# Kernel optimization log

Hardware: AMD Instinct MI355X
Metric: run time of the kernel (lower is better)

The kernel has to match this reference:

```python
import jax, jax.numpy as jnp
import numpy as np

D_MODEL = 1024
N_HEADS = 16
D_K = D_MODEL // N_HEADS


def setup_inputs() -> dict:
    key = jax.random.key(0)
    ks = jax.random.split(key, 12)
    B, S, D, H = 2, 2048, D_MODEL, N_HEADS
    s = 1.0 / np.sqrt(D)
    inp = {
        "x": jax.random.normal(ks[0], (B, S, D), jnp.float32),
        "Wq": jax.random.normal(ks[1], (D, D), jnp.float32) * s,
        "bq": jnp.zeros((D,), jnp.float32),
        "Wk": jax.random.normal(ks[2], (D, D), jnp.float32) * s,
        "bk": jnp.zeros((D,), jnp.float32),
        "Wv": jax.random.normal(ks[3], (D, D), jnp.float32) * s,
        "bv": jnp.zeros((D,), jnp.float32),
        "Wo": jax.random.normal(ks[4], (D, D), jnp.float32) * s,
        "bo": jnp.zeros((D,), jnp.float32),
        "Wp": jax.random.normal(ks[5], (D, H), jnp.float32) * s,
        "bp": jnp.zeros((H,), jnp.float32),
        "alpha": jax.random.normal(ks[6], (H,), jnp.float32) * 0.1,
    }
    return inp


def reference(x, Wq, bq, Wk, bk, Wv, bv, Wo, bo, Wp, bp, alpha):
    B, S, D = x.shape
    H, dk = N_HEADS, D_K
    scale = dk ** -0.5
    # projections -> (B, H, S, dk)
    Q = (x @ Wq + bq).reshape(B, S, H, dk).transpose(0, 2, 1, 3)
    K = (x @ Wk + bk).reshape(B, S, H, dk).transpose(0, 2, 1, 3)
    V = (x @ Wv + bv).reshape(B, S, H, dk).transpose(0, 2, 1, 3)
    scores = jnp.einsum("bhid,bhjd->bhij", Q, K) * scale  # (B,H,S,S)
    # phase derived from x: (B,S,H) -> (B,H,S)
    phase = (x @ Wp + bp).transpose(0, 2, 1)
    # coherence(i,j) = cos(phi_i - phi_j), per batch/head
    coherence = jnp.cos(phase[:, :, :, None] - phase[:, :, None, :])
    scores = scores + alpha[None, :, None, None] * coherence
    attn = jax.nn.softmax(scores, axis=-1)
    out = jnp.einsum("bhij,bhjd->bhid", attn, V)  # (B,H,S,dk)
    out = out.transpose(0, 2, 1, 3).reshape(B, S, D)
    return out @ Wo + bo
```

## Files before the change

kernel.cpp:

```cpp
#include <hip/hip_runtime.h>
#include <math.h>


#define S_LEN 2048
#define NHEADS 16

typedef __attribute__((ext_vector_type(8))) short short8;
typedef __attribute__((ext_vector_type(4))) float floatx4;
typedef __attribute__((ext_vector_type(4))) unsigned int uintx4;

__device__ inline unsigned short f2bf(float f) {
    union { float f; unsigned int i; } v; v.f = f;
    unsigned int u = v.i;
    return (unsigned short)((u + 0x7fffu + ((u >> 16) & 1u)) >> 16);
}
__device__ inline unsigned int pack2_bf16(float hi, float lo) {
    union { float f; unsigned int u; } a, b; a.f = hi; b.f = lo;
    return __builtin_amdgcn_perm(a.u, b.u, 0x07060302u);
}
__device__ inline void async_copy16(const unsigned short* src, unsigned short* dst_lds) {
    __builtin_amdgcn_global_load_lds(
        (const __attribute__((address_space(1))) unsigned int*)(src),
        (__attribute__((address_space(3))) unsigned int*)(dst_lds), 16, 0, 0);
}
__device__ inline void async_copy4(const float* src, float* dst_lds) {
    __builtin_amdgcn_global_load_lds(
        (const __attribute__((address_space(1))) unsigned int*)(src),
        (__attribute__((address_space(3))) unsigned int*)(dst_lds), 4, 0, 0);
}

__global__ __launch_bounds__(256) void transpose4(
    const float* __restrict__ w0, const float* __restrict__ w1,
    const float* __restrict__ w2, const float* __restrict__ w3,
    unsigned short* __restrict__ d0, unsigned short* __restrict__ d1,
    unsigned short* __restrict__ d2, unsigned short* __restrict__ d3) {
    __shared__ __align__(16) unsigned short tile[64][72];
    int bid = blockIdx.x;
    int mat = bid >> 8;
    int tl  = bid & 255;
    int tr = tl >> 4, tc = tl & 15;
    const float* src    = (mat == 0) ? w0 : (mat == 1) ? w1 : (mat == 2) ? w2 : w3;
    unsigned short* dst = (mat == 0) ? d0 : (mat == 1) ? d1 : (mat == 2) ? d2 : d3;
    int t = threadIdx.x;
    int col = t & 63, rbase = (t >> 6) * 16;
#pragma unroll
    for (int i = 0; i < 16; i++) {
        int row = rbase + i;
        tile[row][col] = f2bf(src[(size_t)(tr * 64 + row) * 1024 + tc * 64 + col]);
    }
    __syncthreads();
#pragma unroll
    for (int i = 0; i < 16; i++) {
        int row = rbase + i;
        dst[(size_t)(tc * 64 + row) * 1024 + tr * 64 + col] = tile[col][row];
    }
}

__global__ __launch_bounds__(256) void phase_cvt(
    const float* __restrict__ x, const float* __restrict__ Wp,
    const float* __restrict__ bp,
    float* __restrict__ cosP, float* __restrict__ sinP,
    unsigned short* __restrict__ xb) {
    __shared__ float red[256];
    int bid = blockIdx.x;
    int b = bid >> 11, s = bid & 2047;
    int t = threadIdx.x;
    int h = t & 15, c = t >> 4;
    const float* xr = x + (size_t)bid * 1024;
    {
        float4 xv = *reinterpret_cast<const float4*>(&xr[t * 4]);
        uint2 o;
        o.x = (unsigned int)f2bf(xv.x) | ((unsigned int)f2bf(xv.y) << 16);
        o.y = (unsigned int)f2bf(xv.z) | ((unsigned int)f2bf(xv.w) << 16);
        *reinterpret_cast<uint2*>(&xb[(size_t)bid * 1024 + t * 4]) = o;
    }
    float acc = 0.f;
#pragma unroll 8
    for (int kk = 0; kk < 64; kk++) {
        int k = c * 64 + kk;
        acc += xr[k] * Wp[k * 16 + h];
    }
    red[t] = acc;
    __syncthreads();
    if (t < 16) {
        float sum = 0.f;
#pragma unroll
        for (int c2 = 0; c2 < 16; c2++) sum += red[c2 * 16 + t];
        sum += bp[t];
        float sv, cv;
        __sincosf(sum, &sv, &cv);
        size_t o = ((size_t)b * NHEADS + t) * S_LEN + s;
        cosP[o] = cv; sinP[o] = sv;
    }
}

template <int MT>
__global__ __launch_bounds__(256) void gemm_bt(
    const unsigned short* __restrict__ A, const unsigned short* __restrict__ BT,
    int N, int mode,
    const float* __restrict__ b0, const float* __restrict__ b1,
    const float* __restrict__ b2,
    unsigned short* __restrict__ o0, unsigned short* __restrict__ o1,
    unsigned short* __restrict__ o2, float* __restrict__ of) {
    __shared__ __align__(16) unsigned short As[MT * 32];
    __shared__ __align__(16) unsigned short Bs[128 * 32];
    const int K = 1024;
    const int MI = MT / 32;
    int t = threadIdx.x;
    int mBase = blockIdx.x * MT;
    int nBase = blockIdx.y * 128;
    int w = t >> 6, lane = t & 63, l15 = lane & 15, quad = lane >> 4;
    int wm = (w & 1) * (MT / 2), wn = (w >> 1) * 64;
    floatx4 acc[MI][4];
#pragma unroll
    for (int i = 0; i < MI; i++)
#pragma unroll
        for (int j = 0; j < 4; j++) acc[i][j] = (floatx4){0.f, 0.f, 0.f, 0.f};

    int arow = t >> 2, aseg = (t & 3) * 8;
    for (int k0 = 0; k0 < K; k0 += 32) {
        __syncthreads();
#pragma unroll
        for (int i = 0; i < MT / 64; i++)
            async_copy16(&A[(size_t)(mBase + i * 64 + arow) * K + k0 + aseg],
                         &As[(i * 64 + arow) * 32 + aseg]);
#pragma unroll
        for (int i = 0; i < 2; i++)
            async_copy16(&BT[(size_t)(nBase + i * 64 + arow) * K + k0 + aseg],
                         &Bs[(i * 64 + arow) * 32 + aseg]);
        __syncthreads();
        short8 af[MI], bfr[4];
#pragma unroll
        for (int mi = 0; mi < MI; mi++)
            af[mi] = *reinterpret_cast<const short8*>(&As[(wm + mi * 16 + l15) * 32 + quad * 8]);
#pragma unroll
        for (int ni = 0; ni < 4; ni++)
            bfr[ni] = *reinterpret_cast<const short8*>(&Bs[(wn + ni * 16 + l15) * 32 + quad * 8]);
#pragma unroll
        for (int mi = 0; mi < MI; mi++)
#pragma unroll
            for (int ni = 0; ni < 4; ni++)
                acc[mi][ni] = __builtin_amdgcn_mfma_f32_16x16x32_bf16(af[mi], bfr[ni], acc[mi][ni], 0, 0, 0);
    }

#pragma unroll
    for (int mi = 0; mi < MI; mi++) {
        int rowB = mBase + wm + mi * 16 + quad * 4;
#pragma unroll
        for (int ni = 0; ni < 4; ni++) {
            int col = nBase + wn + ni * 16 + l15;
            if (mode == 0) {
                float bias = b0[col];
#pragma unroll
                for (int r = 0; r < 4; r++) {
                    of[(size_t)(rowB + r) * N + col] = acc[mi][ni][r] + bias;
                }
            } else {
                int mat = col >> 10, nn = col & 1023;
                int h = nn >> 6, d = nn & 63;
                int b = rowB >> 11, sidx = rowB & 2047;
                if (mat == 2) {
                    float bv = b2[nn];
                    unsigned int lo = (unsigned int)f2bf(acc[mi][ni][0] + bv) |
                                      ((unsigned int)f2bf(acc[mi][ni][1] + bv) << 16);
                    unsigned int hi = (unsigned int)f2bf(acc[mi][ni][2] + bv) |
                                      ((unsigned int)f2bf(acc[mi][ni][3] + bv) << 16);
                    *reinterpret_cast<uint2*>(
                        &o2[((size_t)((b * NHEADS + h) * 64 + d)) * S_LEN + sidx]) =
                        make_uint2(lo, hi);
                } else {
                    const float* bias  = (mat == 0) ? b0 : b1;
                    unsigned short* op = (mat == 0) ? o0 : o1;
                    float bv = bias[nn];
                    float scl = (mat == 0) ? 0.18033688f : 1.0f;
#pragma unroll
                    for (int r = 0; r < 4; r++) {
                        float cv = (acc[mi][ni][r] + bv) * scl;
                        op[(((size_t)b * NHEADS + h) * S_LEN + (sidx + r)) * 64 + d] = f2bf(cv);
                    }
                }
            }
        }
    }
}

__global__ __launch_bounds__(256) void vtrans(unsigned int* __restrict__ v) {
    __shared__ unsigned int ld[1024];
    size_t base = (size_t)blockIdx.x * 1024;
    int t = threadIdx.x;
    *reinterpret_cast<uintx4*>(&ld[t * 4]) =
        *reinterpret_cast<const uintx4*>(&v[base + t * 4]);
    __syncthreads();
    int tile = t >> 3, m = t & 7;
    int b = ((m >> 2) << 4) + ((m & 3) << 1);
    const unsigned int* tb = &ld[tile * 32];
    unsigned int a0 = tb[b], a1 = tb[b + 1], h0 = tb[b + 8], h1 = tb[b + 9];
    uintx4 o;
    o[0] = __builtin_amdgcn_perm(h0, a0, 0x05040100u);
    o[1] = __builtin_amdgcn_perm(h0, a0, 0x07060302u);
    o[2] = __builtin_amdgcn_perm(h1, a1, 0x05040100u);
    o[3] = __builtin_amdgcn_perm(h1, a1, 0x07060302u);
    *reinterpret_cast<uintx4*>(&v[base + t * 4]) = o;
}

__global__ __launch_bounds__(256) void attn_kernel(
    const unsigned short* __restrict__ Qg, const unsigned short* __restrict__ Kg,
    const unsigned short* __restrict__ VTg,
    const float* __restrict__ cosP, const float* __restrict__ sinP,
    const float* __restrict__ alpha, unsigned short* __restrict__ ctx) {
    __shared__ __align__(16) unsigned short KsB[2][64 * 64];
    __shared__ __align__(16) unsigned short VtB[2][64 * 64];
    __shared__ __align__(16) float csB[2][128];
    __shared__ __align__(16) unsigned short Plb[4][32 * 72];

    int bid = blockIdx.x;
    int bh = bid >> 4, qt = bid & 15;
    int t = threadIdx.x, w = t >> 6, lane = t & 63, l15 = lane & 15, quad = lane >> 4;
    int m0 = qt * 128 + w * 32;
    size_t base = (size_t)bh * (S_LEN * 64);
    size_t phBase = (size_t)bh * S_LEN;
    const float L2E = 1.44269504f;

    int sj = t >> 3, sg = t & 7;
    int srot = ((sg - (sj & 7)) & 7) * 8;

    short8 qf[2][2];
#pragma unroll
    for (int mi = 0; mi < 2; mi++)
#pragma unroll
        for (int c = 0; c < 2; c++)
            qf[mi][c] = *reinterpret_cast<const short8*>(
                &Qg[base + (size_t)(m0 + mi * 16 + l15) * 64 + c * 32 + quad * 8]);

    float alph = alpha[bh & 15] * L2E;
    float ci[2][4], si[2][4];
#pragma unroll
    for (int mi = 0; mi < 2; mi++)
#pragma unroll
        for (int r = 0; r < 4; r++) {
            size_t o = phBase + m0 + mi * 16 + quad * 4 + r;
            ci[mi][r] = alph * cosP[o];
            si[mi][r] = alph * sinP[o];
        }

    {
        async_copy16(&Kg[base + (size_t)(0 * 64 + sj) * 64 + srot], &KsB[0][t * 8]);
        async_copy16(&Kg[base + (size_t)(0 * 64 + sj + 32) * 64 + srot], &KsB[0][2048 + t * 8]);
        async_copy16(&VTg[base + (size_t)sj * S_LEN + 0 * 64 + srot], &VtB[0][t * 8]);
        async_copy16(&VTg[base + (size_t)(sj + 32) * S_LEN + 0 * 64 + srot], &VtB[0][2048 + t * 8]);
        if (w == 0)      async_copy4(&cosP[phBase + 0 * 64 + lane], &csB[0][lane]);
        else if (w == 1) async_copy4(&sinP[phBase + 0 * 64 + lane], &csB[0][64 + lane]);
    }

    floatx4 oacc[2][4], lacc[2];
#pragma unroll
    for (int mi = 0; mi < 2; mi++) {
#pragma unroll
        for (int tt = 0; tt < 4; tt++) oacc[mi][tt] = (floatx4){0.f, 0.f, 0.f, 0.f};
        lacc[mi] = (floatx4){0.f, 0.f, 0.f, 0.f};
    }
    const short8 ones8 = {(short)0x3F80, (short)0x3F80, (short)0x3F80, (short)0x3F80,
                          (short)0x3F80, (short)0x3F80, (short)0x3F80, (short)0x3F80};

    int rot = l15 & 7;
    int cb0 = 16 * ((quad + rot) & 7);
    int cb1 = 16 * ((quad + 4 + rot) & 7);

    for (int kt = 0; kt < 32; kt++) {
        int p = kt & 1;
        __syncthreads();
        if (kt < 31) {
            int kn = kt + 1, pn = p ^ 1;
            async_copy16(&Kg[base + (size_t)(kn * 64 + sj) * 64 + srot], &KsB[pn][t * 8]);
            async_copy16(&Kg[base + (size_t)(kn * 64 + sj + 32) * 64 + srot], &KsB[pn][2048 + t * 8]);
            async_copy16(&VTg[base + (size_t)sj * S_LEN + kn * 64 + srot], &VtB[pn][t * 8]);
            async_copy16(&VTg[base + (size_t)(sj + 32) * S_LEN + kn * 64 + srot], &VtB[pn][2048 + t * 8]);
            if (w == 0)      async_copy4(&cosP[phBase + kn * 64 + lane], &csB[pn][lane]);
            else if (w == 1) async_copy4(&sinP[phBase + kn * 64 + lane], &csB[pn][64 + lane]);
        }

        floatx4 st[2][4];
#pragma unroll
        for (int jt = 0; jt < 4; jt++) {
            const char* kr = (const char*)&KsB[p][(jt * 16 + l15) * 64];
            short8 kf0 = *reinterpret_cast<const short8*>(kr + cb0);
            short8 kf1 = *reinterpret_cast<const short8*>(kr + cb1);
#pragma unroll
            for (int mi = 0; mi < 2; mi++) {
                floatx4 s = (floatx4){0.f, 0.f, 0.f, 0.f};
                s = __builtin_amdgcn_mfma_f32_16x16x32_bf16(qf[mi][0], kf0, s, 0, 0, 0);
                s = __builtin_amdgcn_mfma_f32_16x16x32_bf16(qf[mi][1], kf1, s, 0, 0, 0);
                st[mi][jt] = s;
            }
        }

        float cjv[4], sjv[4];
#pragma unroll
        for (int jt = 0; jt < 4; jt++) {
            cjv[jt] = csB[p][jt * 16 + l15];
            sjv[jt] = csB[p][64 + jt * 16 + l15];
        }

        unsigned int* pl = reinterpret_cast<unsigned int*>(&Plb[w][0]);
#pragma unroll
        for (int mi = 0; mi < 2; mi++)
#pragma unroll
            for (int r = 0; r < 4; r++) {
                float cc = ci[mi][r], ss = si[mi][r];
                float p0 = __builtin_amdgcn_exp2f(st[mi][0][r] + cc * cjv[0] + ss * sjv[0]);
                float p1 = __builtin_amdgcn_exp2f(st[mi][1][r] + cc * cjv[1] + ss * sjv[1]);
                float p2 = __builtin_amdgcn_exp2f(st[mi][2][r] + cc * cjv[2] + ss * sjv[2]);
                float p3 = __builtin_amdgcn_exp2f(st[mi][3][r] + cc * cjv[3] + ss * sjv[3]);
                int row = mi * 16 + quad * 4 + r;
                pl[row * 36 + l15]      = pack2_bf16(p1, p0);
                pl[row * 36 + 16 + l15] = pack2_bf16(p3, p2);
            }

        short8 pf[2][2];
#pragma unroll
        for (int mi = 0; mi < 2; mi++)
#pragma unroll
            for (int c = 0; c < 2; c++)
                pf[mi][c] = *reinterpret_cast<const short8*>(
                    &Plb[w][(mi * 16 + l15) * 72 + c * 32 + quad * 8]);

#pragma unroll
        for (int c = 0; c < 2; c++) {
            int cb = c ? cb1 : cb0;
#pragma unroll
            for (int tt = 0; tt < 4; tt++) {
                const char* vr = (const char*)&VtB[p][(tt * 16 + l15) * 64];
                short8 vf = *reinterpret_cast<const short8*>(vr + cb);
                oacc[0][tt] = __builtin_amdgcn_mfma_f32_16x16x32_bf16(pf[0][c], vf, oacc[0][tt], 0, 0, 0);
                oacc[1][tt] = __builtin_amdgcn_mfma_f32_16x16x32_bf16(pf[1][c], vf, oacc[1][tt], 0, 0, 0);
            }
            lacc[0] = __builtin_amdgcn_mfma_f32_16x16x32_bf16(pf[0][c], ones8, lacc[0], 0, 0, 0);
            lacc[1] = __builtin_amdgcn_mfma_f32_16x16x32_bf16(pf[1][c], ones8, lacc[1], 0, 0, 0);
        }
    }

    int b = bh >> 4, h = bh & 15;
#pragma unroll
    for (int mi = 0; mi < 2; mi++) {
        float inv[4];
#pragma unroll
        for (int r = 0; r < 4; r++) inv[r] = 1.0f / lacc[mi][r];
#pragma unroll
        for (int tt = 0; tt < 4; tt++)
#pragma unroll
            for (int r = 0; r < 4; r++) {
                int srow = m0 + mi * 16 + quad * 4 + r;
                ctx[((size_t)(b * S_LEN + srow)) * 1024 + h * 64 + tt * 16 + l15] =
                    f2bf(oacc[mi][tt][r] * inv[r]);
            }
    }
}

extern "C" void kernel_launch(void* const* d_in, const int* in_sizes, int n_in,
                              void* d_out, int out_size, void* d_ws, size_t ws_size,
                              hipStream_t stream) {
    const float* x     = (const float*)d_in[0];
    const float* Wq    = (const float*)d_in[1];
    const float* bq    = (const float*)d_in[2];
    const float* Wk    = (const float*)d_in[3];
    const float* bk    = (const float*)d_in[4];
    const float* Wv    = (const float*)d_in[5];
    const float* bv    = (const float*)d_in[6];
    const float* Wo    = (const float*)d_in[7];
    const float* bo    = (const float*)d_in[8];
    const float* Wp    = (const float*)d_in[9];
    const float* bp    = (const float*)d_in[10];
    const float* alpha = (const float*)d_in[11];
    float* out = (float*)d_out;

    const size_t MB = 1048576;
    char* ws = (char*)d_ws;
    unsigned short* WT   = (unsigned short*)(ws);
    unsigned short* WoT  = (unsigned short*)(ws + 6 * MB);
    unsigned short* xb   = (unsigned short*)(ws + 8 * MB);
    unsigned short* ctx  = (unsigned short*)(ws + 8 * MB);
    unsigned short* Qw   = (unsigned short*)(ws + 16 * MB);
    unsigned short* Kw   = (unsigned short*)(ws + 24 * MB);
    unsigned short* VTg  = (unsigned short*)(ws + 32 * MB);
    float* cosP          = (float*)(ws + 40 * MB);
    float* sinP          = (float*)(ws + 40 * MB + 262144);

    transpose4<<<dim3(1024), dim3(256), 0, stream>>>(
        Wq, Wk, Wv, Wo, WT, WT + 1048576, WT + 2097152, WoT);
    phase_cvt<<<dim3(4096), dim3(256), 0, stream>>>(
        x, Wp, bp, cosP, sinP, xb);
    gemm_bt<128><<<dim3(32, 24), dim3(256), 0, stream>>>(
        xb, WT, 3072, 1, bq, bk, bv, Qw, Kw, VTg, (float*)nullptr);
    vtrans<<<dim3(2048), dim3(256), 0, stream>>>((unsigned int*)VTg);
    attn_kernel<<<dim3(512), dim3(256), 0, stream>>>(
        Qw, Kw, VTg, cosP, sinP, alpha, ctx);
    gemm_bt<64><<<dim3(64, 8), dim3(256), 0, stream>>>(
        ctx, WoT, 1024, 0, bo, bo, bo,
        (unsigned short*)nullptr, (unsigned short*)nullptr,
        (unsigned short*)nullptr, out);
}
```

Before: 242.5 us.

## Merge prep kernels, fold V permutation into GEMM epilogue, widen attention blocks

Combines the weight transpose and phase/convert kernels into one launch split by block index. The vtrans pass is removed, and the QKV GEMM epilogue now writes V directly in the permuted interleaved layout, using scalar 2-byte stores instead of packed 8-byte stores. The attention kernel moves to 512 threads per block with 8 waves of 16 query rows each instead of 4 waves of 32. This halves per-thread registers and the per-thread async copy count but doubles K/V fragment reads from LDS per query row. The aims are fewer launches, no extra pass over V, and higher occupancy in attention; the cost is scattered V stores and less K/V reuse per wave.

```diff
diff --git a/kernel.cpp b/kernel.cpp
--- a/kernel.cpp
+++ b/kernel.cpp
@@ -29,68 +29,68 @@
         (__attribute__((address_space(3))) unsigned int*)(dst_lds), 4, 0, 0);
 }
 
-__global__ __launch_bounds__(256) void transpose4(
+__global__ __launch_bounds__(256) void prep_kernel(
+    const float* __restrict__ x, const float* __restrict__ Wp,
+    const float* __restrict__ bp,
     const float* __restrict__ w0, const float* __restrict__ w1,
     const float* __restrict__ w2, const float* __restrict__ w3,
     unsigned short* __restrict__ d0, unsigned short* __restrict__ d1,
-    unsigned short* __restrict__ d2, unsigned short* __restrict__ d3) {
-    __shared__ __align__(16) unsigned short tile[64][72];
-    int bid = blockIdx.x;
-    int mat = bid >> 8;
-    int tl  = bid & 255;
-    int tr = tl >> 4, tc = tl & 15;
-    const float* src    = (mat == 0) ? w0 : (mat == 1) ? w1 : (mat == 2) ? w2 : w3;
-    unsigned short* dst = (mat == 0) ? d0 : (mat == 1) ? d1 : (mat == 2) ? d2 : d3;
-    int t = threadIdx.x;
-    int col = t & 63, rbase = (t >> 6) * 16;
-#pragma unroll
-    for (int i = 0; i < 16; i++) {
-        int row = rbase + i;
-        tile[row][col] = f2bf(src[(size_t)(tr * 64 + row) * 1024 + tc * 64 + col]);
-    }
-    __syncthreads();
-#pragma unroll
-    for (int i = 0; i < 16; i++) {
-        int row = rbase + i;
-        dst[(size_t)(tc * 64 + row) * 1024 + tr * 64 + col] = tile[col][row];
-    }
-}
-
-__global__ __launch_bounds__(256) void phase_cvt(
-    const float* __restrict__ x, const float* __restrict__ Wp,
-    const float* __restrict__ bp,
+    unsigned short* __restrict__ d2, unsigned short* __restrict__ d3,
     float* __restrict__ cosP, float* __restrict__ sinP,
     unsigned short* __restrict__ xb) {
-    __shared__ float red[256];
-    int bid = blockIdx.x;
-    int b = bid >> 11, s = bid & 2047;
+    __shared__ __align__(16) unsigned short shmem[64 * 72];
     int t = threadIdx.x;
-    int h = t & 15, c = t >> 4;
-    const float* xr = x + (size_t)bid * 1024;
-    {
-        float4 xv = *reinterpret_cast<const float4*>(&xr[t * 4]);
-        uint2 o;
-        o.x = (unsigned int)f2bf(xv.x) | ((unsigned int)f2bf(xv.y) << 16);
-        o.y = (unsigned int)f2bf(xv.z) | ((unsigned int)f2bf(xv.w) << 16);
-        *reinterpret_cast<uint2*>(&xb[(size_t)bid * 1024 + t * 4]) = o;
-    }
-    float acc = 0.f;
+    if (blockIdx.x < 4096) {
+        float* red = reinterpret_cast<float*>(shmem);
+        int bid = blockIdx.x;
+        int b = bid >> 11, s = bid & 2047;
+        int h = t & 15, c = t >> 4;
+        const float* xr = x + (size_t)bid * 1024;
+        {
+            float4 xv = *reinterpret_cast<const float4*>(&xr[t * 4]);
+            uint2 o;
+            o.x = (unsigned int)f2bf(xv.x) | ((unsigned int)f2bf(xv.y) << 16);
+            o.y = (unsigned int)f2bf(xv.z) | ((unsigned int)f2bf(xv.w) << 16);
+            *reinterpret_cast<uint2*>(&xb[(size_t)bid * 1024 + t * 4]) = o;
+        }
+        float acc = 0.f;
 #pragma unroll 8
-    for (int kk = 0; kk < 64; kk++) {
-        int k = c * 64 + kk;
-        acc += xr[k] * Wp[k * 16 + h];
-    }
-    red[t] = acc;
-    __syncthreads();
-    if (t < 16) {
-        float sum = 0.f;
-#pragma unroll
-        for (int c2 = 0; c2 < 16; c2++) sum += red[c2 * 16 + t];
-        sum += bp[t];
-        float sv, cv;
-        __sincosf(sum, &sv, &cv);
-        size_t o = ((size_t)b * NHEADS + t) * S_LEN + s;
-        cosP[o] = cv; sinP[o] = sv;
+        for (int kk = 0; kk < 64; kk++) {
+            int k = c * 64 + kk;
+            acc += xr[k] * Wp[k * 16 + h];
+        }
+        red[t] = acc;
+        __syncthreads();
+        if (t < 16) {
+            float sum = 0.f;
+#pragma unroll
+            for (int c2 = 0; c2 < 16; c2++) sum += red[c2 * 16 + t];
+            sum += bp[t];
+            float sv, cv;
+            __sincosf(sum, &sv, &cv);
+            size_t o = ((size_t)b * NHEADS + t) * S_LEN + s;
+            cosP[o] = cv; sinP[o] = sv;
+        }
+    } else {
+        unsigned short (*tile)[72] = reinterpret_cast<unsigned short (*)[72]>(shmem);
+        int bid = blockIdx.x - 4096;
+        int mat = bid >> 8;
+        int tl  = bid & 255;
+        int tr = tl >> 4, tc = tl & 15;
+        const float* src    = (mat == 0) ? w0 : (mat == 1) ? w1 : (mat == 2) ? w2 : w3;
+        unsigned short* dst = (mat == 0) ? d0 : (mat == 1) ? d1 : (mat == 2) ? d2 : d3;
+        int col = t & 63, rbase = (t >> 6) * 16;
+#pragma unroll
+        for (int i = 0; i < 16; i++) {
+            int row = rbase + i;
+            tile[row][col] = f2bf(src[(size_t)(tr * 64 + row) * 1024 + tc * 64 + col]);
+        }
+        __syncthreads();
+#pragma unroll
+        for (int i = 0; i < 16; i++) {
+            int row = rbase + i;
+            dst[(size_t)(tc * 64 + row) * 1024 + tr * 64 + col] = tile[col][row];
+        }
     }
 }
 
@@ -161,13 +161,13 @@
                 int b = rowB >> 11, sidx = rowB & 2047;
                 if (mat == 2) {
                     float bv = b2[nn];
-                    unsigned int lo = (unsigned int)f2bf(acc[mi][ni][0] + bv) |
-                                      ((unsigned int)f2bf(acc[mi][ni][1] + bv) << 16);
-                    unsigned int hi = (unsigned int)f2bf(acc[mi][ni][2] + bv) |
-                                      ((unsigned int)f2bf(acc[mi][ni][3] + bv) << 16);
-                    *reinterpret_cast<uint2*>(
-                        &o2[((size_t)((b * NHEADS + h) * 64 + d)) * S_LEN + sidx]) =
-                        make_uint2(lo, hi);
+                    int jj = sidx & 63;
+                    int a2 = jj >> 5, c2 = (jj >> 4) & 1, bb = jj & 15;
+                    size_t rowOff = ((size_t)((b * NHEADS + h) * 64 + d)) * S_LEN +
+                                    (sidx & ~63) + a2 * 32 + c2;
+#pragma unroll
+                    for (int r = 0; r < 4; r++)
+                        o2[rowOff + 2 * (bb + r)] = f2bf(acc[mi][ni][r] + bv);
                 } else {
                     const float* bias  = (mat == 0) ? b0 : b1;
                     unsigned short* op = (mat == 0) ? o0 : o1;
@@ -184,26 +184,7 @@
     }
 }
 
-__global__ __launch_bounds__(256) void vtrans(unsigned int* __restrict__ v) {
-    __shared__ unsigned int ld[1024];
-    size_t base = (size_t)blockIdx.x * 1024;
-    int t = threadIdx.x;
-    *reinterpret_cast<uintx4*>(&ld[t * 4]) =
-        *reinterpret_cast<const uintx4*>(&v[base + t * 4]);
-    __syncthreads();
-    int tile = t >> 3, m = t & 7;
-    int b = ((m >> 2) << 4) + ((m & 3) << 1);
-    const unsigned int* tb = &ld[tile * 32];
-    unsigned int a0 = tb[b], a1 = tb[b + 1], h0 = tb[b + 8], h1 = tb[b + 9];
-    uintx4 o;
-    o[0] = __builtin_amdgcn_perm(h0, a0, 0x05040100u);
-    o[1] = __builtin_amdgcn_perm(h0, a0, 0x07060302u);
-    o[2] = __builtin_amdgcn_perm(h1, a1, 0x05040100u);
-    o[3] = __builtin_amdgcn_perm(h1, a1, 0x07060302u);
-    *reinterpret_cast<uintx4*>(&v[base + t * 4]) = o;
-}
-
-__global__ __launch_bounds__(256) void attn_kernel(
+__global__ __launch_bounds__(512) void attn_kernel(
     const unsigned short* __restrict__ Qg, const unsigned short* __restrict__ Kg,
     const unsigned short* __restrict__ VTg,
     const float* __restrict__ cosP, const float* __restrict__ sinP,
@@ -211,12 +192,12 @@
     __shared__ __align__(16) unsigned short KsB[2][64 * 64];
     __shared__ __align__(16) unsigned short VtB[2][64 * 64];
     __shared__ __align__(16) float csB[2][128];
-    __shared__ __align__(16) unsigned short Plb[4][32 * 72];
+    __shared__ __align__(16) unsigned short Plb[8][16 * 72];
 
     int bid = blockIdx.x;
     int bh = bid >> 4, qt = bid & 15;
     int t = threadIdx.x, w = t >> 6, lane = t & 63, l15 = lane & 15, quad = lane >> 4;
-    int m0 = qt * 128 + w * 32;
+    int m0 = qt * 128 + w * 16;
     size_t base = (size_t)bh * (S_LEN * 64);
     size_t phBase = (size_t)bh * S_LEN;
     const float L2E = 1.44269504f;
@@ -224,41 +205,32 @@
     int sj = t >> 3, sg = t & 7;
     int srot = ((sg - (sj & 7)) & 7) * 8;
 
-    short8 qf[2][2];
-#pragma unroll
-    for (int mi = 0; mi < 2; mi++)
-#pragma unroll
-        for (int c = 0; c < 2; c++)
-            qf[mi][c] = *reinterpret_cast<const short8*>(
-                &Qg[base + (size_t)(m0 + mi * 16 + l15) * 64 + c * 32 + quad * 8]);
+    short8 qf[2];
+#pragma unroll
+    for (int c = 0; c < 2; c++)
+        qf[c] = *reinterpret_cast<const short8*>(
+            &Qg[base + (size_t)(m0 + l15) * 64 + c * 32 + quad * 8]);
 
     float alph = alpha[bh & 15] * L2E;
-    float ci[2][4], si[2][4];
-#pragma unroll
-    for (int mi = 0; mi < 2; mi++)
-#pragma unroll
-        for (int r = 0; r < 4; r++) {
-            size_t o = phBase + m0 + mi * 16 + quad * 4 + r;
-            ci[mi][r] = alph * cosP[o];
-            si[mi][r] = alph * sinP[o];
-        }
+    float ci[4], si[4];
+#pragma unroll
+    for (int r = 0; r < 4; r++) {
+        size_t o = phBase + m0 + quad * 4 + r;
+        ci[r] = alph * cosP[o];
+        si[r] = alph * sinP[o];
+    }
 
     {
-        async_copy16(&Kg[base + (size_t)(0 * 64 + sj) * 64 + srot], &KsB[0][t * 8]);
-        async_copy16(&Kg[base + (size_t)(0 * 64 + sj + 32) * 64 + srot], &KsB[0][2048 + t * 8]);
-        async_copy16(&VTg[base + (size_t)sj * S_LEN + 0 * 64 + srot], &VtB[0][t * 8]);
-        async_copy16(&VTg[base + (size_t)(sj + 32) * S_LEN + 0 * 64 + srot], &VtB[0][2048 + t * 8]);
-        if (w == 0)      async_copy4(&cosP[phBase + 0 * 64 + lane], &csB[0][lane]);
-        else if (w == 1) async_copy4(&sinP[phBase + 0 * 64 + lane], &csB[0][64 + lane]);
-    }
-
-    floatx4 oacc[2][4], lacc[2];
-#pragma unroll
-    for (int mi = 0; mi < 2; mi++) {
-#pragma unroll
-        for (int tt = 0; tt < 4; tt++) oacc[mi][tt] = (floatx4){0.f, 0.f, 0.f, 0.f};
-        lacc[mi] = (floatx4){0.f, 0.f, 0.f, 0.f};
-    }
+        async_copy16(&Kg[base + (size_t)sj * 64 + srot], &KsB[0][t * 8]);
+        async_copy16(&VTg[base + (size_t)sj * S_LEN + srot], &VtB[0][t * 8]);
+        if (w == 2)      async_copy4(&cosP[phBase + lane], &csB[0][lane]);
+        else if (w == 3) async_copy4(&sinP[phBase + lane], &csB[0][64 + lane]);
+    }
+
+    floatx4 oacc[4], lacc;
+#pragma unroll
+    for (int tt = 0; tt < 4; tt++) oacc[tt] = (floatx4){0.f, 0.f, 0.f, 0.f};
+    lacc = (floatx4){0.f, 0.f, 0.f, 0.f};
     const short8 ones8 = {(short)0x3F80, (short)0x3F80, (short)0x3F80, (short)0x3F80,
                           (short)0x3F80, (short)0x3F80, (short)0x3F80, (short)0x3F80};
 
@@ -272,26 +244,21 @@
         if (kt < 31) {
             int kn = kt + 1, pn = p ^ 1;
             async_copy16(&Kg[base + (size_t)(kn * 64 + sj) * 64 + srot], &KsB[pn][t * 8]);
-            async_copy16(&Kg[base + (size_t)(kn * 64 + sj + 32) * 64 + srot], &KsB[pn][2048 + t * 8]);
             async_copy16(&VTg[base + (size_t)sj * S_LEN + kn * 64 + srot], &VtB[pn][t * 8]);
-            async_copy16(&VTg[base + (size_t)(sj + 32) * S_LEN + kn * 64 + srot], &VtB[pn][2048 + t * 8]);
-            if (w == 0)      async_copy4(&cosP[phBase + kn * 64 + lane], &csB[pn][lane]);
-            else if (w == 1) async_copy4(&sinP[phBase + kn * 64 + lane], &csB[pn][64 + lane]);
-        }
-
-        floatx4 st[2][4];
+            if (w == 2)      async_copy4(&cosP[phBase + kn * 64 + lane], &csB[pn][lane]);
+            else if (w == 3) async_copy4(&sinP[phBase + kn * 64 + lane], &csB[pn][64 + lane]);
+        }
+
+        floatx4 st[4];
 #pragma unroll
         for (int jt = 0; jt < 4; jt++) {
             const char* kr = (const char*)&KsB[p][(jt * 16 + l15) * 64];
             short8 kf0 = *reinterpret_cast<const short8*>(kr + cb0);
             short8 kf1 = *reinterpret_cast<const short8*>(kr + cb1);
-#pragma unroll
-            for (int mi = 0; mi < 2; mi++) {
-                floatx4 s = (floatx4){0.f, 0.f, 0.f, 0.f};
-                s = __builtin_amdgcn_mfma_f32_16x16x32_bf16(qf[mi][0], kf0, s, 0, 0, 0);
-                s = __builtin_amdgcn_mfma_f32_16x16x32_bf16(qf[mi][1], kf1, s, 0, 0, 0);
-                st[mi][jt] = s;
-            }
+            floatx4 s = (floatx4){0.f, 0.f, 0.f, 0.f};
+            s = __builtin_amdgcn_mfma_f32_16x16x32_bf16(qf[0], kf0, s, 0, 0, 0);
+            s = __builtin_amdgcn_mfma_f32_16x16x32_bf16(qf[1], kf1, s, 0, 0, 0);
+            st[jt] = s;
         }
 
         float cjv[4], sjv[4];
@@ -303,26 +270,22 @@
 
         unsigned int* pl = reinterpret_cast<unsigned int*>(&Plb[w][0]);
 #pragma unroll
-        for (int mi = 0; mi < 2; mi++)
-#pragma unroll
-            for (int r = 0; r < 4; r++) {
-                float cc = ci[mi][r], ss = si[mi][r];
-                float p0 = __builtin_amdgcn_exp2f(st[mi][0][r] + cc * cjv[0] + ss * sjv[0]);
-                float p1 = __builtin_amdgcn_exp2f(st[mi][1][r] + cc * cjv[1] + ss * sjv[1]);
-                float p2 = __builtin_amdgcn_exp2f(st[mi][2][r] + cc * cjv[2] + ss * sjv[2]);
-                float p3 = __builtin_amdgcn_exp2f(st[mi][3][r] + cc * cjv[3] + ss * sjv[3]);
-                int row = mi * 16 + quad * 4 + r;
-                pl[row * 36 + l15]      = pack2_bf16(p1, p0);
-                pl[row * 36 + 16 + l15] = pack2_bf16(p3, p2);
-            }
-
-        short8 pf[2][2];
-#pragma unroll
-        for (int mi = 0; mi < 2; mi++)
-#pragma unroll
-            for (int c = 0; c < 2; c++)
-                pf[mi][c] = *reinterpret_cast<const short8*>(
-                    &Plb[w][(mi * 16 + l15) * 72 + c * 32 + quad * 8]);
+        for (int r = 0; r < 4; r++) {
+            float cc = ci[r], ss = si[r];
+            float p0 = __builtin_amdgcn_exp2f(st[0][r] + cc * cjv[0] + ss * sjv[0]);
+            float p1 = __builtin_amdgcn_exp2f(st[1][r] + cc * cjv[1] + ss * sjv[1]);
+            float p2 = __builtin_amdgcn_exp2f(st[2][r] + cc * cjv[2] + ss * sjv[2]);
+            float p3 = __builtin_amdgcn_exp2f(st[3][r] + cc * cjv[3] + ss * sjv[3]);
+            int row = quad * 4 + r;
+            pl[row * 36 + l15]      = pack2_bf16(p1, p0);
+            pl[row * 36 + 16 + l15] = pack2_bf16(p3, p2);
+        }
+
+        short8 pf[2];
+#pragma unroll
+        for (int c = 0; c < 2; c++)
+            pf[c] = *reinterpret_cast<const short8*>(
+                &Plb[w][l15 * 72 + c * 32 + quad * 8]);
 
 #pragma unroll
         for (int c = 0; c < 2; c++) {
@@ -331,29 +294,24 @@
             for (int tt = 0; tt < 4; tt++) {
                 const char* vr = (const char*)&VtB[p][(tt * 16 + l15) * 64];
                 short8 vf = *reinterpret_cast<const short8*>(vr + cb);
-                oacc[0][tt] = __builtin_amdgcn_mfma_f32_16x16x32_bf16(pf[0][c], vf, oacc[0][tt], 0, 0, 0);
-                oacc[1][tt] = __builtin_amdgcn_mfma_f32_16x16x32_bf16(pf[1][c], vf, oacc[1][tt], 0, 0, 0);
+                oacc[tt] = __builtin_amdgcn_mfma_f32_16x16x32_bf16(pf[c], vf, oacc[tt], 0, 0, 0);
             }
-            lacc[0] = __builtin_amdgcn_mfma_f32_16x16x32_bf16(pf[0][c], ones8, lacc[0], 0, 0, 0);
-            lacc[1] = __builtin_amdgcn_mfma_f32_16x16x32_bf16(pf[1][c], ones8, lacc[1], 0, 0, 0);
+            lacc = __builtin_amdgcn_mfma_f32_16x16x32_bf16(pf[c], ones8, lacc, 0, 0, 0);
         }
     }
 
     int b = bh >> 4, h = bh & 15;
-#pragma unroll
-    for (int mi = 0; mi < 2; mi++) {
-        float inv[4];
-#pragma unroll
-        for (int r = 0; r < 4; r++) inv[r] = 1.0f / lacc[mi][r];
-#pragma unroll
-        for (int tt = 0; tt < 4; tt++)
-#pragma unroll
-            for (int r = 0; r < 4; r++) {
-                int srow = m0 + mi * 16 + quad * 4 + r;
-                ctx[((size_t)(b * S_LEN + srow)) * 1024 + h * 64 + tt * 16 + l15] =
-                    f2bf(oacc[mi][tt][r] * inv[r]);
-            }
-    }
+    float inv[4];
+#pragma unroll
+    for (int r = 0; r < 4; r++) inv[r] = 1.0f / lacc[r];
+#pragma unroll
+    for (int tt = 0; tt < 4; tt++)
+#pragma unroll
+        for (int r = 0; r < 4; r++) {
+            int srow = m0 + quad * 4 + r;
+            ctx[((size_t)(b * S_LEN + srow)) * 1024 + h * 64 + tt * 16 + l15] =
+                f2bf(oacc[tt][r] * inv[r]);
+        }
 }
 
 extern "C" void kernel_launch(void* const* d_in, const int* in_sizes, int n_in,
@@ -385,14 +343,12 @@
     float* cosP          = (float*)(ws + 40 * MB);
     float* sinP          = (float*)(ws + 40 * MB + 262144);
 
-    transpose4<<<dim3(1024), dim3(256), 0, stream>>>(
-        Wq, Wk, Wv, Wo, WT, WT + 1048576, WT + 2097152, WoT);
-    phase_cvt<<<dim3(4096), dim3(256), 0, stream>>>(
-        x, Wp, bp, cosP, sinP, xb);
+    prep_kernel<<<dim3(5120), dim3(256), 0, stream>>>(
+        x, Wp, bp, Wq, Wk, Wv, Wo,
+        WT, WT + 1048576, WT + 2097152, WoT, cosP, sinP, xb);
     gemm_bt<128><<<dim3(32, 24), dim3(256), 0, stream>>>(
         xb, WT, 3072, 1, bq, bk, bv, Qw, Kw, VTg, (float*)nullptr);
-    vtrans<<<dim3(2048), dim3(256), 0, stream>>>((unsigned int*)VTg);
-    attn_kernel<<<dim3(512), dim3(256), 0, stream>>>(
+    attn_kernel<<<dim3(512), dim3(512), 0, stream>>>(
         Qw, Kw, VTg, cosP, sinP, alpha, ctx);
     gemm_bt<64><<<dim3(64, 8), dim3(256), 0, stream>>>(
         ctx, WoT, 1024, 0, bo, bo, bo,
```

New measurement: 221.2 us. 1.1x faster.
